# Kernel optimization log

Hardware: AMD Instinct MI355X
Metric: run time of the kernel (lower is better)

## Reference

```python
import jax, jax.numpy as jnp
import numpy as np

SEQ, B, OBS, H = 128, 256, 64, 1024

def setup_inputs() -> dict:
    key = jax.random.key(0)
    ks = jax.random.split(key, 16)
    s = 0.03  # keep weights small so tanh/sigmoid stay in a sane range
    n = lambda k, shape, sc=s: jax.random.normal(k, shape, jnp.float32) * sc
    return {
        "x": jax.random.normal(ks[0], (SEQ * B, OBS), jnp.float32),
        "done": jax.random.randint(ks[1], (SEQ * B,), 0, 2).astype(jnp.int32),
        "h0": n(ks[2], (2, B, H), 0.1),
        "c0": n(ks[3], (2, B, H), 0.1),
        "W_ih0": n(ks[4], (4 * H, OBS)),
        "W_hh0": n(ks[5], (4 * H, H)),
        "b_ih0": jnp.zeros((4 * H,), jnp.float32),
        "b_hh0": jnp.zeros((4 * H,), jnp.float32),
        "W_ih1": n(ks[6], (4 * H, H)),
        "W_hh1": n(ks[7], (4 * H, H)),
        "b_ih1": jnp.zeros((4 * H,), jnp.float32),
        "b_hh1": jnp.zeros((4 * H,), jnp.float32),
        "ln_g": jnp.ones((H,), jnp.float32),
        "ln_b": jnp.zeros((H,), jnp.float32),
        "W1": n(ks[8], (512, H)),
        "b1": jnp.zeros((512,), jnp.float32),
        "W2": n(ks[9], (128, 512)),
        "b2": jnp.zeros((128,), jnp.float32),
        "W3": n(ks[10], (64, 128)),
        "b3": jnp.zeros((64,), jnp.float32),
        "Wv": n(ks[11], (1, 64)),
        "bv": jnp.zeros((1,), jnp.float32),
    }

def _lstm_cell(xin, h, c, Wih, Whh, bih, bhh):
    # PyTorch gate order: input, forget, cell(g), output
    g = xin @ Wih.T + bih + h @ Whh.T + bhh
    i, f, gg, o = jnp.split(g, 4, axis=-1)
    c2 = jax.nn.sigmoid(f) * c + jax.nn.sigmoid(i) * jnp.tanh(gg)
    h2 = jax.nn.sigmoid(o) * jnp.tanh(c2)
    return h2, c2

def reference(x, done, h0, c0, W_ih0, W_hh0, b_ih0, b_hh0, W_ih1, W_hh1,
              b_ih1, b_hh1, ln_g, ln_b, W1, b1, W2, b2, W3, b3, Wv, bv):
    batch = h0.shape[1]
    obs = x.shape[-1]
    xs = x.reshape(-1, batch, obs)                      # (S, B, obs)
    ds = done.reshape(-1, batch).astype(x.dtype)        # (S, B)

    def step(carry, td):
        h, c = carry                                    # each (2, B, H)
        xt, dt = td
        m = (1.0 - dt)[:, None]                         # reset mask (B, 1)
        h0_, c0_ = _lstm_cell(xt, h[0] * m, c[0] * m, W_ih0, W_hh0, b_ih0, b_hh0)
        h1_, c1_ = _lstm_cell(h0_, h[1] * m, c[1] * m, W_ih1, W_hh1, b_ih1, b_hh1)
        return (jnp.stack([h0_, h1_]), jnp.stack([c0_, c1_])), h1_

    (hN, cN), hs = jax.lax.scan(step, (h0, c0), (xs, ds))
    hidden = hs.reshape(-1, hs.shape[-1])               # (S*B, H)

    # LayerNorm (eps = 1e-5, torch default)
    mu = hidden.mean(-1, keepdims=True)
    var = jnp.mean(jnp.square(hidden - mu), -1, keepdims=True)
    hn = (hidden - mu) * jax.lax.rsqrt(var + 1e-5) * ln_g + ln_b

    a = jax.nn.elu(hn @ W1.T + b1)
    a = jax.nn.elu(a @ W2.T + b2)
    a = jax.nn.elu(a @ W3.T + b3)
    value = a @ Wv.T + bv                               # (S*B, 1)
    return value, hN, cN
```

## Files before the change

### kernel.cpp

```cpp
#include <hip/hip_runtime.h>
#include <cstdint>
#include <cstddef>

typedef unsigned short u16;
typedef __attribute__((ext_vector_type(8))) short short8;
typedef __attribute__((ext_vector_type(4))) float f32x4;

#define SEQ 128
#define BATCH 256
#define HID 1024
#define LSZ 262144

#define MFMA(a,b,c) __builtin_amdgcn_mfma_f32_16x16x32_bf16((a),(b),(c),0,0,0)

__device__ __forceinline__ u16 f2b(float f) {
  union { float f; unsigned u; } v; v.f = f;
  unsigned r = (v.u + 0x7FFFu + ((v.u >> 16) & 1u)) >> 16;
  return (u16)r;
}
__device__ __forceinline__ float b2f(u16 h) {
  union { unsigned u; float f; } v; v.u = ((unsigned)h) << 16; return v.f;
}
__device__ __forceinline__ float sigm(float x){ return 1.f/(1.f + __expf(-x)); }
__device__ __forceinline__ float tanh_f(float x){
  x = fminf(15.f, fmaxf(-15.f, x));
  float e = __expf(2.f*x); return (e-1.f)/(e+1.f);
}
__device__ __forceinline__ float eluf(float x){ return x > 0.f ? x : expm1f(x); }

__device__ __forceinline__ void gload(const u16* p, short8& d) {
  asm volatile("global_load_dwordx4 %0, %1, off" : "=&v"(d) : "v"(p) : "memory");
}
__device__ __forceinline__ void gload_nt(const u16* p, short8& d) {
  asm volatile("global_load_dwordx4 %0, %1, off nt" : "=&v"(d) : "v"(p) : "memory");
}
__device__ __forceinline__ void gload_cg(const u16* p, short8& d) {
  asm volatile("global_load_dwordx4 %0, %1, off sc0 sc1 nt" : "=&v"(d) : "v"(p) : "memory");
}
__device__ __forceinline__ void store_cg(u16* p, short8 v) {
  asm volatile("global_store_dwordx4 %0, %1, off sc0 sc1 nt" :: "v"(p), "v"(v) : "memory");
}
__device__ __forceinline__ void wait_vm0() {
  asm volatile("s_waitcnt vmcnt(0)" ::: "memory");
}
__device__ __forceinline__ void waitgroup(int* f, int tgt) {
  if (threadIdx.x < 64) {
    int idx = threadIdx.x & 31;
    while (__hip_atomic_load(f + idx, __ATOMIC_RELAXED, __HIP_MEMORY_SCOPE_AGENT) < tgt)
      __builtin_amdgcn_s_sleep(1);
  }
  __syncthreads();
}

#define TIES_VB(vB) "+v"(vB[0][0]),"+v"(vB[0][1]),"+v"(vB[0][2]),"+v"(vB[0][3]), \
                    "+v"(vB[1][0]),"+v"(vB[1][1]),"+v"(vB[1][2]),"+v"(vB[1][3]), \
                    "+v"(vB[2][0]),"+v"(vB[2][1]),"+v"(vB[2][2]),"+v"(vB[2][3]), \
                    "+v"(vB[3][0]),"+v"(vB[3][1]),"+v"(vB[3][2]),"+v"(vB[3][3])
#define TIES_SV "+v"(sv[0]),"+v"(sv[1]),"+v"(sv[2]),"+v"(sv[3]),"+v"(sv[4]),"+v"(sv[5]),"+v"(sv[6]),"+v"(sv[7])

static const size_t OFF_W0F  = 0;
static const size_t OFF_W1F  = 8912896;
static const size_t OFF_XF   = 25690112;
static const size_t OFF_H0U  = 29884416;
static const size_t OFF_C0   = 30932992;
static const size_t OFF_C1   = 31981568;
static const size_t OFF_H1U  = 33030144;
static const size_t OFF_BS0  = 100663296;
static const size_t OFF_BS1  = 100679680;
static const size_t OFF_FLG  = 100696064;
static const size_t OFF_MU   = 100697088;
static const size_t OFF_RSTD = 100828160;
static const size_t OFF_W1LN = 100959232;
static const size_t OFF_S1   = 102007808;
static const size_t OFF_B1P  = 102009856;
static const size_t OFF_W2B  = 102011904;
static const size_t OFF_W3B  = 102142976;
static const size_t OFF_A1   = 102159360;
static const size_t OFF_A2   = 0;
static const size_t OFF_A3   = 8912896;

__global__ void prep_wf(const float* __restrict__ wih, const float* __restrict__ whh,
                        u16* __restrict__ out, int nkb, int kx) {
  int b = blockIdx.x; int cg = b >> 3, ct = b & 7;
  int g = ct >> 1;
  int n = nkb << 9;
  for (int e = threadIdx.x; e < n; e += 256) {
    int kb = e >> 9, r = e & 511;
    int q = r >> 7, col16 = (r >> 3) & 15, j = r & 7;
    int hl = (ct & 1) * 16 + col16;
    int gr = g * HID + cg * 32 + hl;
    int k = kb * 32 + q * 8 + j;
    float w = (k < kx) ? wih[(size_t)gr * kx + k] : whh[(size_t)gr * HID + (k - kx)];
    out[((size_t)(cg * nkb + kb) * 8 + ct) * 512 + r] = f2b(w);
  }
}

__global__ void prep_w1ln(const float* __restrict__ w1, const float* __restrict__ lng,
                          const float* __restrict__ lnb, const float* __restrict__ b1,
                          u16* __restrict__ w1ln, float* __restrict__ S1, float* __restrict__ b1p) {
  int j = blockIdx.x;
  float s = 0.f, bb = 0.f;
  for (int k = threadIdx.x; k < HID; k += 256) {
    float w = w1[(size_t)j * HID + k];
    u16 q = f2b(w * lng[k]);
    w1ln[(size_t)j * HID + k] = q;
    s += b2f(q);
    bb += w * lnb[k];
  }
  __shared__ float r1[256], r2[256];
  r1[threadIdx.x] = s; r2[threadIdx.x] = bb;
  __syncthreads();
  for (int o = 128; o > 0; o >>= 1) {
    if (threadIdx.x < (unsigned)o) { r1[threadIdx.x] += r1[threadIdx.x+o]; r2[threadIdx.x] += r2[threadIdx.x+o]; }
    __syncthreads();
  }
  if (threadIdx.x == 0) { S1[j] = r1[0]; b1p[j] = b1[j] + r2[0]; }
}

__global__ void prep_misc(const float* bih0, const float* bhh0, const float* bih1, const float* bhh1,
                          const float* x, const float* h0in, const float* c0in,
                          const float* w2, const float* w3,
                          float* bs0, float* bs1, u16* xf, u16* h0u, u16* h1u,
                          float* c0buf, float* c1buf, u16* w2b, u16* w3b, int* flg) {
  size_t i = (size_t)blockIdx.x * blockDim.x + threadIdx.x;
  if (i < 4096) { bs0[i] = bih0[i] + bhh0[i]; return; }
  i -= 4096;
  if (i < 4096) { bs1[i] = bih1[i] + bhh1[i]; return; }
  i -= 4096;
  if (i < 2097152) {
    int o = (int)i;
    int r = o & 511, tile = o >> 9;
    int q = r >> 7, rl = (r >> 3) & 15, j = r & 7;
    int kb = tile & 1, v = tile >> 1;
    int grt = v & 15, t = v >> 4;
    int row = grt * 16 + rl, k = kb * 32 + q * 8 + j;
    xf[o] = f2b(x[((size_t)t * BATCH + row) * 64 + k]);
    return;
  }
  i -= 2097152;
  if (i < 262144) {
    int o = (int)i;
    int r = o & 511, tile = o >> 9;
    int q = r >> 7, rl = (r >> 3) & 15, j = r & 7;
    int grt = tile >> 5, kb = tile & 31;
    int row = grt * 16 + rl, h = kb * 32 + q * 8 + j;
    h0u[o] = f2b(h0in[(size_t)row * HID + h]);
    return;
  }
  i -= 262144;
  if (i < 262144) {
    int o = (int)i;
    int r = o & 511, tile = o >> 9;
    int q = r >> 7, rl = (r >> 3) & 15, j = r & 7;
    int grt = tile >> 5, kb = tile & 31;
    int row = grt * 16 + rl, h = kb * 32 + q * 8 + j;
    h1u[o] = f2b(h0in[LSZ + (size_t)row * HID + h]);
    return;
  }
  i -= 262144;
  if (i < LSZ) { c0buf[i] = c0in[i]; return; }
  i -= LSZ;
  if (i < LSZ) { c1buf[i] = c0in[LSZ + i]; return; }
  i -= LSZ;
  if (i < 65536) { w2b[i] = f2b(w2[i]); return; }
  i -= 65536;
  if (i < 8192) { w3b[i] = f2b(w3[i]); return; }
  i -= 8192;
  if (i < 256) { flg[i] = 0; return; }
}

__global__ __launch_bounds__(256, 1) void lstm_persist(
    const u16* __restrict__ w0f, const u16* __restrict__ w1f, const u16* __restrict__ xf,
    u16* __restrict__ h0u, u16* __restrict__ h1u,
    float* __restrict__ c0b, float* __restrict__ c1b,
    const float* __restrict__ bs0, const float* __restrict__ bs1,
    const int* __restrict__ done, int* __restrict__ flg,
    float* __restrict__ dout)
{
  const int bid = blockIdx.x;
  const int layer = bid >> 7;
  const int rg = (bid >> 5) & 3;
  const int cg = bid & 31;
  const int tid = threadIdx.x;
  const int lane = tid & 63, wv = tid >> 6;
  const int wgr = wv & 1, wgc = wv >> 1;
  const int quad = lane >> 4, c16 = lane & 15;
  const int NKB = layer ? 64 : 34;
  const int NC  = layer ? 8 : 5;
  const int NH  = layer ? 16 : 9;
  const u16* Wf = layer ? w1f : w0f;
  const float* bs = layer ? bs1 : bs0;
  float* cb = layer ? c1b : c0b;
  int* fl0 = flg;
  int* fl1 = flg + 128;
  int* myf = (layer ? fl1 : fl0) + rg * 32 + cg;
  int* g0 = fl0 + rg * 32;
  int* g1 = fl1 + rg * 32;

  __shared__ __align__(16) u16 smem[32768];
  float* gl = (float*)smem;

  const int sgrt = rg * 4 + wv;
  const int woff = (lane >> 4) * 128 + (lane & 15) * 8;
  const int srow = rg * 64 + wv * 16 + (lane & 15);
  const short8 z8 = {0,0,0,0,0,0,0,0};

  float creg[8];
  {
    const float* cp0 = cb + (size_t)(rg * 64 + (tid >> 2)) * HID + cg * 32 + (tid & 3) * 8;
    #pragma unroll
    for (int j = 0; j < 8; ++j) creg[j] = cp0[j];
  }

  for (int t = 0; t < SEQ; ++t) {
    if (layer == 0) {
      if (t >= 1) waitgroup(g0, t);
      if (t >= 2) waitgroup(g1, t - 1);
    } else {
      waitgroup(g0, t + 1);
      if (t >= 1) waitgroup(g1, t);
    }

    int sdone = done[t * BATCH + srow];
    asm volatile("" : "+v"(sdone));

    f32x4 acc0[4], acc1[4];
    #pragma unroll
    for (int i = 0; i < 4; ++i) { acc0[i] = (f32x4){0,0,0,0}; acc1[i] = (f32x4){0,0,0,0}; }
    short8 sv[8];
    short8 vBa[4][4], vBb[4][4];

    auto issueA = [&](int c) {
      int kb0 = c * 8;
      #pragma unroll
      for (int kbl = 0; kbl < 8; ++kbl) {
        int kb = kb0 + kbl;
        if (kb > NKB - 1) kb = NKB - 1;
        if (layer == 0) {
          if (kb < 2) {
            gload_nt(xf + ((size_t)((t * 16 + sgrt) * 2 + kb)) * 512 + woff, sv[kbl]);
          } else {
            gload_cg(h0u + (size_t)(t & 1) * 262144 + (size_t)(sgrt * 32 + (kb - 2)) * 512 + woff, sv[kbl]);
          }
        } else {
          if (kb < 32) {
            gload_cg(h0u + (size_t)((t + 1) & 1) * 262144 + (size_t)(sgrt * 32 + kb) * 512 + woff, sv[kbl]);
          } else {
            gload_nt(h1u + (size_t)t * 262144 + (size_t)(sgrt * 32 + (kb - 32)) * 512 + woff, sv[kbl]);
          }
        }
      }
    };
    auto commitA = [&](int c) {
      int kb0 = c * 8;
      int bo = (c & 1) << 14;
      u16* d = &smem[bo + wv * 512 + woff];
      #pragma unroll
      for (int kbl = 0; kbl < 8; ++kbl) {
        int kb = kb0 + kbl;
        int maskable = layer ? (kb >= 32) : (kb >= 2);
        short8 v = sv[kbl];
        if (maskable && sdone) v = z8;
        *(short8*)(d + kbl * 2048) = v;
      }
    };
    auto issueB = [&](int h, short8 (&vB)[4][4]) {
      int kk = h * 4;
      #pragma unroll
      for (int kbl = 0; kbl < 4; ++kbl) {
        int kbx = kk + kbl;
        if (kbx > NKB - 1) kbx = NKB - 1;
        #pragma unroll
        for (int ct = 0; ct < 4; ++ct)
          gload(Wf + ((size_t)(cg * NKB + kbx) * 8 + wgc * 4 + ct) * 512 + lane * 8, vB[kbl][ct]);
      }
    };
    auto comp4 = [&](int h, short8 (&vB)[4][4]) {
      int kbc4 = NKB - h * 4; if (kbc4 > 4) kbc4 = 4;
      int bo = ((h >> 1) & 1) << 14;
      int tb = (h & 1) * 4;
      #pragma unroll
      for (int kbl = 0; kbl < 4; ++kbl) if (kbl < kbc4) {
        short8 af0 = *(const short8*)&smem[bo + ((tb + kbl) * 4 + wgr * 2 + 0) * 512 + lane * 8];
        short8 af1 = *(const short8*)&smem[bo + ((tb + kbl) * 4 + wgr * 2 + 1) * 512 + lane * 8];
        #pragma unroll
        for (int ct = 0; ct < 4; ++ct) {
          acc0[ct] = MFMA(af0, vB[kbl][ct], acc0[ct]);
          acc1[ct] = MFMA(af1, vB[kbl][ct], acc1[ct]);
        }
      }
    };

    issueB(0, vBa);
    issueA(0);
    issueB(1, vBb);
    asm volatile("s_waitcnt vmcnt(16)" : TIES_SV, TIES_VB(vBa) :: "memory");
    __builtin_amdgcn_sched_barrier(0);
    commitA(0);
    __syncthreads();

    for (int c = 0; c < NC - 1; ++c) {
      issueA(c + 1);
      comp4(2 * c, vBa);
      issueB(2 * c + 2, vBa);
      asm volatile("s_waitcnt vmcnt(24)" : TIES_VB(vBb) :: "memory");
      __builtin_amdgcn_sched_barrier(0);
      comp4(2 * c + 1, vBb);
      issueB(2 * c + 3, vBb);
      asm volatile("s_waitcnt vmcnt(32)" : TIES_SV :: "memory");
      __builtin_amdgcn_sched_barrier(0);
      commitA(c + 1);
      asm volatile("s_waitcnt vmcnt(16)" : TIES_VB(vBa) :: "memory");
      __builtin_amdgcn_sched_barrier(0);
      __syncthreads();
    }
    {
      int c = NC - 1;
      comp4(2 * c, vBa);
      asm volatile("s_waitcnt vmcnt(0)" : TIES_VB(vBb) :: "memory");
      __builtin_amdgcn_sched_barrier(0);
      if (2 * c + 1 < NH) comp4(2 * c + 1, vBb);
      __syncthreads();
    }

    #pragma unroll
    for (int ct = 0; ct < 4; ++ct)
      #pragma unroll
      for (int rgi = 0; rgi < 4; ++rgi) {
        int row0 = wgr * 32 + quad * 4 + rgi;
        int col = wgc * 64 + ct * 16 + c16;
        gl[row0 * 128 + col] = acc0[ct][rgi];
        gl[(row0 + 16) * 128 + col] = acc1[ct][rgi];
      }
    __syncthreads();

    {
      int row = tid >> 2;
      int q = tid & 3;
      int h8 = q * 8;
      int rowg = rg * 64 + row;
      int H0 = cg * 32 + h8;
      const float* glp = gl + row * 128;
      float m = done[t * BATCH + rowg] ? 0.f : 1.f;
      short8 hv;
      float h2a[8];
      #pragma unroll
      for (int j = 0; j < 8; ++j) {
        float ivv = glp[h8 + j]      + bs[H0 + j];
        float fvv = glp[32 + h8 + j] + bs[HID + H0 + j];
        float gvv = glp[64 + h8 + j] + bs[2*HID + H0 + j];
        float ovv = glp[96 + h8 + j] + bs[3*HID + H0 + j];
        float c2 = sigm(fvv) * (creg[j] * m) + sigm(ivv) * tanh_f(gvv);
        float h2 = sigm(ovv) * tanh_f(c2);
        creg[j] = c2;
        h2a[j] = h2;
        ((u16*)&hv)[j] = f2b(h2);
      }
      size_t off = (size_t)((rg * 4 + (row >> 4)) * 32 + cg) * 512 + (size_t)(q * 16 + (row & 15)) * 8;
      if (layer == 0) store_cg(h0u + (size_t)((t + 1) & 1) * 262144 + off, hv);
      else            store_cg(h1u + (size_t)(t + 1) * 262144 + off, hv);
      if (t == SEQ - 1) {
        float* dh = dout + 32768 + (size_t)layer * LSZ + (size_t)rowg * HID + H0;
        float* dc = dout + 32768 + 2 * LSZ + (size_t)layer * LSZ + (size_t)rowg * HID + H0;
        #pragma unroll
        for (int j = 0; j < 8; ++j) { dh[j] = h2a[j]; dc[j] = creg[j]; }
      }
    }
    wait_vm0();
    __syncthreads();
    if (tid == 0) __hip_atomic_fetch_add(myf, 1, __ATOMIC_RELAXED, __HIP_MEMORY_SCOPE_AGENT);
  }
}

__global__ void ln_stats(const u16* __restrict__ h1u, float* __restrict__ mu, float* __restrict__ rstd) {
  int R = blockIdx.x * 4 + (threadIdx.x >> 6);
  int l = threadIdx.x & 63;
  int t = R >> 8, brow = R & 255, grt = brow >> 4, rl = brow & 15;
  const u16* base = h1u + (size_t)(t + 1) * 262144 + (size_t)(grt * 32 + (l >> 1)) * 512;
  int q2 = (l & 1) * 2;
  short8 v0 = *(const short8*)(base + (q2 * 16 + rl) * 8);
  short8 v1 = *(const short8*)(base + ((q2 + 1) * 16 + rl) * 8);
  float s = 0.f, q = 0.f;
  #pragma unroll
  for (int e = 0; e < 8; ++e) {
    float a = b2f((u16)v0[e]); s += a; q += a*a;
    float b = b2f((u16)v1[e]); s += b; q += b*b;
  }
  for (int o = 32; o > 0; o >>= 1) { s += __shfl_xor(s, o); q += __shfl_xor(q, o); }
  if (l == 0) {
    float mm = s * (1.f/1024.f);
    float var = q * (1.f/1024.f) - mm*mm;
    mu[R] = mm; rstd[R] = rsqrtf(var + 1e-5f);
  }
}

__global__ __launch_bounds__(512, 4) void mlp_gemm(
    const u16* __restrict__ A, int lda, int amode,
    const u16* __restrict__ B, int K, int N,
    u16* __restrict__ out, int ldo, int mode, int swiz,
    const float* __restrict__ mu, const float* __restrict__ rstd,
    const float* __restrict__ S1v, const float* __restrict__ bias)
{
  int nt, mtb;
  if (swiz) { int p = blockIdx.x * gridDim.y + blockIdx.y; nt = p & 3; mtb = p >> 2; }
  else { nt = blockIdx.x; mtb = blockIdx.y; }
  const int tid = threadIdx.x, lane = tid & 63, wv = tid >> 6;
  const int quad = lane >> 4, c16 = lane & 15;
  __shared__ __align__(16) u16 Am[16384], Bm[16384];
  f32x4 acc[8];
  #pragma unroll
  for (int i = 0; i < 8; ++i) acc[i] = (f32x4){0.f,0.f,0.f,0.f};

  int arow[4], akl[4], bcol[4];
  #pragma unroll
  for (int i = 0; i < 4; ++i) {
    int s = tid + i * 512, sub = s >> 6, lp = s & 63;
    int ks = sub >> 3, u = sub & 7;
    arow[i] = mtb * 128 + u * 16 + (lp & 15);
    akl[i]  = ks * 32 + (lp >> 4) * 8;
    bcol[i] = nt * 128 + u * 16 + (lp & 15);
  }
  short8 vA[4], vB[4];
  const short8 z8 = {0,0,0,0,0,0,0,0};
  const int NCH = K >> 7;
  auto load_stage = [&](int ci) {
    int kc = ci << 7;
    #pragma unroll
    for (int i = 0; i < 4; ++i) {
      if (amode) {
        int R = arow[i], k = kc + akl[i];
        const u16* p = A + (size_t)((R >> 8) + 1) * 262144
                         + (size_t)(((R >> 4) & 15) * 32 + (k >> 5)) * 512
                         + (size_t)((((k >> 3) & 3) * 16 + (R & 15)) * 8);
        vA[i] = *(const short8*)p;
      } else {
        vA[i] = *(const short8*)(A + (size_t)arow[i] * lda + kc + akl[i]);
      }
      vB[i] = (bcol[i] < N) ? *(const short8*)(B + (size_t)bcol[i] * K + kc + akl[i]) : z8;
    }
  };
  load_stage(0);
  for (int ci = 0; ci < NCH; ++ci) {
    #pragma unroll
    for (int i = 0; i < 4; ++i) {
      *(short8*)&Am[(size_t)(tid + i*512) * 8] = vA[i];
      *(short8*)&Bm[(size_t)(tid + i*512) * 8] = vB[i];
    }
    __syncthreads();
    if (ci + 1 < NCH) load_stage(ci + 1);
    #pragma unroll
    for (int ks = 0; ks < 4; ++ks) {
      short8 bf = *(const short8*)&Bm[((ks*8 + wv)*64 + lane) * 8];
      #pragma unroll
      for (int rt = 0; rt < 8; ++rt) {
        short8 af = *(const short8*)&Am[((ks*8 + rt)*64 + lane) * 8];
        acc[rt] = MFMA(af, bf, acc[rt]);
      }
    }
    __syncthreads();
  }
  int col = nt * 128 + wv * 16 + c16;
  if (col < N) {
    #pragma unroll
    for (int rt = 0; rt < 8; ++rt) {
      #pragma unroll
      for (int rgi = 0; rgi < 4; ++rgi) {
        int row = mtb * 128 + rt * 16 + quad * 4 + rgi;
        float v = acc[rt][rgi];
        if (mode == 0) v = v * rstd[row] - mu[row] * rstd[row] * S1v[col] + bias[col];
        else           v = v + bias[col];
        v = eluf(v);
        out[(size_t)row * ldo + col] = f2b(v);
      }
    }
  }
}

__global__ void value_head(const u16* __restrict__ a3, const float* __restrict__ wv,
                           const float* __restrict__ bv, float* __restrict__ dout) {
  int row = blockIdx.x * 256 + threadIdx.x;
  const short8* p = (const short8*)(a3 + (size_t)row * 64);
  float s = bv[0];
  #pragma unroll
  for (int j = 0; j < 8; ++j) {
    short8 v = p[j];
    #pragma unroll
    for (int e = 0; e < 8; ++e) s += b2f((u16)v[e]) * wv[j*8+e];
  }
  dout[row] = s;
}

extern "C" void kernel_launch(void* const* d_in, const int* in_sizes, int n_in,
                              void* d_out, int out_size, void* d_ws, size_t ws_size,
                              hipStream_t stream) {
  (void)in_sizes; (void)n_in; (void)out_size; (void)ws_size;
  const float* x    = (const float*)d_in[0];
  const int*   done = (const int*)d_in[1];
  const float* h0in = (const float*)d_in[2];
  const float* c0in = (const float*)d_in[3];
  const float* wih0 = (const float*)d_in[4];
  const float* whh0 = (const float*)d_in[5];
  const float* bih0 = (const float*)d_in[6];
  const float* bhh0 = (const float*)d_in[7];
  const float* wih1 = (const float*)d_in[8];
  const float* whh1 = (const float*)d_in[9];
  const float* bih1 = (const float*)d_in[10];
  const float* bhh1 = (const float*)d_in[11];
  const float* lng  = (const float*)d_in[12];
  const float* lnb  = (const float*)d_in[13];
  const float* w1   = (const float*)d_in[14];
  const float* b1   = (const float*)d_in[15];
  const float* w2   = (const float*)d_in[16];
  const float* b2   = (const float*)d_in[17];
  const float* w3   = (const float*)d_in[18];
  const float* b3   = (const float*)d_in[19];
  const float* wvp  = (const float*)d_in[20];
  const float* bvp  = (const float*)d_in[21];
  float* dout = (float*)d_out;
  char* ws = (char*)d_ws;

  u16*   w0f  = (u16*)(ws + OFF_W0F);
  u16*   w1f  = (u16*)(ws + OFF_W1F);
  u16*   xf   = (u16*)(ws + OFF_XF);
  u16*   h0u  = (u16*)(ws + OFF_H0U);
  u16*   h1u  = (u16*)(ws + OFF_H1U);
  float* c0b  = (float*)(ws + OFF_C0);
  float* c1b  = (float*)(ws + OFF_C1);
  float* bs0  = (float*)(ws + OFF_BS0);
  float* bs1  = (float*)(ws + OFF_BS1);
  int*   flg  = (int*)(ws + OFF_FLG);
  float* mu   = (float*)(ws + OFF_MU);
  float* rstd = (float*)(ws + OFF_RSTD);
  u16*   w1ln = (u16*)(ws + OFF_W1LN);
  float* s1   = (float*)(ws + OFF_S1);
  float* b1p  = (float*)(ws + OFF_B1P);
  u16*   w2b  = (u16*)(ws + OFF_W2B);
  u16*   w3b  = (u16*)(ws + OFF_W3B);
  u16*   a1   = (u16*)(ws + OFF_A1);
  u16*   a2   = (u16*)(ws + OFF_A2);
  u16*   a3   = (u16*)(ws + OFF_A3);

  prep_wf<<<256, 256, 0, stream>>>(wih0, whh0, w0f, 34, 64);
  prep_wf<<<256, 256, 0, stream>>>(wih1, whh1, w1f, 64, 1024);
  prep_w1ln<<<512, 256, 0, stream>>>(w1, lng, lnb, b1, w1ln, s1, b1p);
  prep_misc<<<12609, 256, 0, stream>>>(bih0, bhh0, bih1, bhh1, x, h0in, c0in, w2, w3,
                                       bs0, bs1, xf, h0u, h1u, c0b, c1b, w2b, w3b, flg);

  lstm_persist<<<256, 256, 0, stream>>>(w0f, w1f, xf, h0u, h1u, c0b, c1b,
                                        bs0, bs1, done, flg, dout);

  ln_stats<<<8192, 256, 0, stream>>>(h1u, mu, rstd);
  mlp_gemm<<<dim3(8, 128), 512, 0, stream>>>(h1u, 0, 1, w1ln, 1024, 512, a1, 512, 0, 1, mu, rstd, s1, b1p);
  mlp_gemm<<<dim3(1, 256), 512, 0, stream>>>(a1, 512, 0, w2b, 512, 128, a2, 128, 1, 0, mu, rstd, s1, b2);
  mlp_gemm<<<dim3(1, 256), 512, 0, stream>>>(a2, 128, 0, w3b, 128, 64, a3, 64, 1, 0, mu, rstd, s1, b3);
  value_head<<<128, 256, 0, stream>>>(a3, wvp, bvp, dout);
}
```

Measured before the change: 3.365 ms.

## Rework inter-block flag sync and reorder layer-1 K chunks to overlap waiting

New measurement: 3.127 ms. 7.1% less time.

```diff
diff --git a/kernel.cpp b/kernel.cpp
--- a/kernel.cpp
+++ b/kernel.cpp
@@ -35,19 +35,27 @@
   asm volatile("global_load_dwordx4 %0, %1, off nt" : "=&v"(d) : "v"(p) : "memory");
 }
 __device__ __forceinline__ void gload_cg(const u16* p, short8& d) {
-  asm volatile("global_load_dwordx4 %0, %1, off sc0 sc1 nt" : "=&v"(d) : "v"(p) : "memory");
+  asm volatile("global_load_dwordx4 %0, %1, off sc0 sc1" : "=&v"(d) : "v"(p) : "memory");
 }
 __device__ __forceinline__ void store_cg(u16* p, short8 v) {
-  asm volatile("global_store_dwordx4 %0, %1, off sc0 sc1 nt" :: "v"(p), "v"(v) : "memory");
+  asm volatile("global_store_dwordx4 %0, %1, off sc0 sc1" :: "v"(p), "v"(v) : "memory");
 }
 __device__ __forceinline__ void wait_vm0() {
   asm volatile("s_waitcnt vmcnt(0)" ::: "memory");
 }
-__device__ __forceinline__ void waitgroup(int* f, int tgt) {
-  if (threadIdx.x < 64) {
-    int idx = threadIdx.x & 31;
-    while (__hip_atomic_load(f + idx, __ATOMIC_RELAXED, __HIP_MEMORY_SCOPE_AGENT) < tgt)
+__device__ __forceinline__ void flag_set(int* p, int val) {
+  asm volatile("global_store_dword %0, %1, off sc0 sc1" :: "v"(p), "v"(val) : "memory");
+}
+__device__ __forceinline__ void waitgroup(const int* f, int tgt) {
+  if (threadIdx.x < 32) {
+    const int* p = f + threadIdx.x * 32;
+    while (true) {
+      int v;
+      asm volatile("global_load_dword %0, %1, off sc0 sc1\n\ts_waitcnt vmcnt(0)"
+                   : "=v"(v) : "v"(p) : "memory");
+      if (v >= tgt) break;
       __builtin_amdgcn_s_sleep(1);
+    }
   }
   __syncthreads();
 }
@@ -62,12 +70,10 @@
 static const size_t OFF_W1F  = 8912896;
 static const size_t OFF_XF   = 25690112;
 static const size_t OFF_H0U  = 29884416;
-static const size_t OFF_C0   = 30932992;
-static const size_t OFF_C1   = 31981568;
+static const size_t OFF_FLG  = 30932992;
 static const size_t OFF_H1U  = 33030144;
 static const size_t OFF_BS0  = 100663296;
 static const size_t OFF_BS1  = 100679680;
-static const size_t OFF_FLG  = 100696064;
 static const size_t OFF_MU   = 100697088;
 static const size_t OFF_RSTD = 100828160;
 static const size_t OFF_W1LN = 100959232;
@@ -118,10 +124,10 @@
 }
 
 __global__ void prep_misc(const float* bih0, const float* bhh0, const float* bih1, const float* bhh1,
-                          const float* x, const float* h0in, const float* c0in,
+                          const float* x, const float* h0in,
                           const float* w2, const float* w3,
                           float* bs0, float* bs1, u16* xf, u16* h0u, u16* h1u,
-                          float* c0buf, float* c1buf, u16* w2b, u16* w3b, int* flg) {
+                          u16* w2b, u16* w3b, int* flg) {
   size_t i = (size_t)blockIdx.x * blockDim.x + threadIdx.x;
   if (i < 4096) { bs0[i] = bih0[i] + bhh0[i]; return; }
   i -= 4096;
@@ -158,21 +164,17 @@
     return;
   }
   i -= 262144;
-  if (i < LSZ) { c0buf[i] = c0in[i]; return; }
-  i -= LSZ;
-  if (i < LSZ) { c1buf[i] = c0in[LSZ + i]; return; }
-  i -= LSZ;
   if (i < 65536) { w2b[i] = f2b(w2[i]); return; }
   i -= 65536;
   if (i < 8192) { w3b[i] = f2b(w3[i]); return; }
   i -= 8192;
-  if (i < 256) { flg[i] = 0; return; }
+  if (i < 256) { flg[i * 32] = 0; return; }
 }
 
 __global__ __launch_bounds__(256, 1) void lstm_persist(
     const u16* __restrict__ w0f, const u16* __restrict__ w1f, const u16* __restrict__ xf,
     u16* __restrict__ h0u, u16* __restrict__ h1u,
-    float* __restrict__ c0b, float* __restrict__ c1b,
+    const float* __restrict__ c0all,
     const float* __restrict__ bs0, const float* __restrict__ bs1,
     const int* __restrict__ done, int* __restrict__ flg,
     float* __restrict__ dout)
@@ -190,12 +192,12 @@
   const int NH  = layer ? 16 : 9;
   const u16* Wf = layer ? w1f : w0f;
   const float* bs = layer ? bs1 : bs0;
-  float* cb = layer ? c1b : c0b;
+  const float* cb = c0all + (size_t)layer * LSZ;
   int* fl0 = flg;
-  int* fl1 = flg + 128;
-  int* myf = (layer ? fl1 : fl0) + rg * 32 + cg;
-  int* g0 = fl0 + rg * 32;
-  int* g1 = fl1 + rg * 32;
+  int* fl1 = flg + 128 * 32;
+  int* myf = (layer ? fl1 : fl0) + (rg * 32 + cg) * 32;
+  int* g0 = fl0 + rg * 32 * 32;
+  int* g1 = fl1 + rg * 32 * 32;
 
   __shared__ __align__(16) u16 smem[32768];
   float* gl = (float*)smem;
@@ -214,10 +216,9 @@
 
   for (int t = 0; t < SEQ; ++t) {
     if (layer == 0) {
+      if (t >= 2) waitgroup(g1, t - 1);
       if (t >= 1) waitgroup(g0, t);
-      if (t >= 2) waitgroup(g1, t - 1);
     } else {
-      waitgroup(g0, t + 1);
       if (t >= 1) waitgroup(g1, t);
     }
 
@@ -230,8 +231,10 @@
     short8 sv[8];
     short8 vBa[4][4], vBb[4][4];
 
-    auto issueA = [&](int c) {
-      int kb0 = c * 8;
+    auto PC = [&](int lc) { return layer ? ((lc + 4) & 7) : lc; };
+
+    auto issueA = [&](int lc) {
+      int kb0 = PC(lc) * 8;
       #pragma unroll
       for (int kbl = 0; kbl < 8; ++kbl) {
         int kb = kb0 + kbl;
@@ -251,9 +254,9 @@
         }
       }
     };
-    auto commitA = [&](int c) {
-      int kb0 = c * 8;
-      int bo = (c & 1) << 14;
+    auto commitA = [&](int lc) {
+      int kb0 = PC(lc) * 8;
+      int bo = (lc & 1) << 14;
       u16* d = &smem[bo + wv * 512 + woff];
       #pragma unroll
       for (int kbl = 0; kbl < 8; ++kbl) {
@@ -264,8 +267,9 @@
         *(short8*)(d + kbl * 2048) = v;
       }
     };
-    auto issueB = [&](int h, short8 (&vB)[4][4]) {
-      int kk = h * 4;
+    auto issueB = [&](int lh, short8 (&vB)[4][4]) {
+      int ph = layer ? ((lh + 8) & 15) : lh;
+      int kk = ph * 4;
       #pragma unroll
       for (int kbl = 0; kbl < 4; ++kbl) {
         int kbx = kk + kbl;
@@ -275,10 +279,11 @@
           gload(Wf + ((size_t)(cg * NKB + kbx) * 8 + wgc * 4 + ct) * 512 + lane * 8, vB[kbl][ct]);
       }
     };
-    auto comp4 = [&](int h, short8 (&vB)[4][4]) {
-      int kbc4 = NKB - h * 4; if (kbc4 > 4) kbc4 = 4;
-      int bo = ((h >> 1) & 1) << 14;
-      int tb = (h & 1) * 4;
+    auto comp4 = [&](int lh, short8 (&vB)[4][4]) {
+      int ph = layer ? ((lh + 8) & 15) : lh;
+      int kbc4 = NKB - ph * 4; if (kbc4 > 4) kbc4 = 4;
+      int bo = ((lh >> 1) & 1) << 14;
+      int tb = (lh & 1) * 4;
       #pragma unroll
       for (int kbl = 0; kbl < 4; ++kbl) if (kbl < kbc4) {
         short8 af0 = *(const short8*)&smem[bo + ((tb + kbl) * 4 + wgr * 2 + 0) * 512 + lane * 8];
@@ -300,6 +305,7 @@
     __syncthreads();
 
     for (int c = 0; c < NC - 1; ++c) {
+      if (layer && c == 3) waitgroup(g0, t + 1);
       issueA(c + 1);
       comp4(2 * c, vBa);
       issueB(2 * c + 2, vBa);
@@ -368,7 +374,7 @@
     }
     wait_vm0();
     __syncthreads();
-    if (tid == 0) __hip_atomic_fetch_add(myf, 1, __ATOMIC_RELAXED, __HIP_MEMORY_SCOPE_AGENT);
+    if (tid == 0) flag_set(myf, t + 1);
   }
 }
 
@@ -524,8 +530,6 @@
   u16*   xf   = (u16*)(ws + OFF_XF);
   u16*   h0u  = (u16*)(ws + OFF_H0U);
   u16*   h1u  = (u16*)(ws + OFF_H1U);
-  float* c0b  = (float*)(ws + OFF_C0);
-  float* c1b  = (float*)(ws + OFF_C1);
   float* bs0  = (float*)(ws + OFF_BS0);
   float* bs1  = (float*)(ws + OFF_BS1);
   int*   flg  = (int*)(ws + OFF_FLG);
@@ -543,10 +547,10 @@
   prep_wf<<<256, 256, 0, stream>>>(wih0, whh0, w0f, 34, 64);
   prep_wf<<<256, 256, 0, stream>>>(wih1, whh1, w1f, 64, 1024);
   prep_w1ln<<<512, 256, 0, stream>>>(w1, lng, lnb, b1, w1ln, s1, b1p);
-  prep_misc<<<12609, 256, 0, stream>>>(bih0, bhh0, bih1, bhh1, x, h0in, c0in, w2, w3,
-                                       bs0, bs1, xf, h0u, h1u, c0b, c1b, w2b, w3b, flg);
-
-  lstm_persist<<<256, 256, 0, stream>>>(w0f, w1f, xf, h0u, h1u, c0b, c1b,
+  prep_misc<<<12609, 256, 0, stream>>>(bih0, bhh0, bih1, bhh1, x, h0in, w2, w3,
+                                       bs0, bs1, xf, h0u, h1u, w2b, w3b, flg);
+
+  lstm_persist<<<256, 256, 0, stream>>>(w0f, w1f, xf, h0u, h1u, c0in,
                                         bs0, bs1, done, flg, dout);
 
   ln_stats<<<8192, 256, 0, stream>>>(h1u, mu, rstd);
```
